# Kernel optimization log

Hardware: AMD Instinct MI355X
Metric: run time of the kernel (lower is better)

## Reference

```python
import jax, jax.numpy as jnp
import numpy as np

L = 8      # num_layers (experts)
N = 8192   # tokens
H = 768    # hidden_dim
I = 1536   # inner = hidden_dim * expansion (2.0)


def setup_inputs() -> dict:
    key = jax.random.key(0)
    k = jax.random.split(key, 6)
    s1 = 1.0 / np.sqrt(H)  # torch nn.Linear default init bound (fan_in)
    s2 = 1.0 / np.sqrt(I)
    return {
        "z": jax.random.normal(k[0], (N, H), dtype=jnp.float32),
        "layer_ids": jax.random.randint(k[1], (N,), 0, L),
        "w1": jax.random.uniform(k[2], (L, H, I), jnp.float32, -s1, s1),
        "b1": jax.random.uniform(k[3], (L, I), jnp.float32, -s1, s1),
        "w2": jax.random.uniform(k[4], (L, I, H), jnp.float32, -s2, s2),
        "b2": jax.random.uniform(k[5], (L, H), jnp.float32, -s2, s2),
    }


def reference(z, layer_ids, w1, b1, w2, b2):
    # Per-token expert MLP: out[n] = z[n] + MLP_{layer_ids[n]}(z[n]).
    # Dense-all-experts formulation (jit-safe, no data-dependent shapes):
    # run every expert on all tokens, then gather each token's own expert row.
    h = jnp.einsum('nh,lhi->lni', z, w1) + b1[:, None, :]       # [L, N, I]
    a = jax.nn.gelu(h, approximate=False)                        # exact erf GELU (torch default)
    y = jnp.einsum('lni,lih->lnh', a, w2) + b2[:, None, :]       # [L, N, H]
    sel = y[layer_ids, jnp.arange(z.shape[0])]                   # [N, H] pick each token's expert
    return z + sel
```

## Files before the change

### kernel.cpp

```cpp
#include <hip/hip_runtime.h>
#include <cstdint>
#include <cstddef>

#define LNUM 8
#define NTOK 8192
#define HDIM 768
#define IDIM 1536

typedef __bf16 bf16x8 __attribute__((ext_vector_type(8)));
typedef float f32x4 __attribute__((ext_vector_type(4)));

__device__ __forceinline__ void gload16(void* lds, const void* gsrc) {
  __builtin_amdgcn_global_load_lds(
      (const __attribute__((address_space(1))) void*)gsrc,
      (__attribute__((address_space(3))) void*)lds, 16, 0, 0);
}

__device__ __forceinline__ float gelu_f(float x) {
  float xx = x * x;
  float u = x * __builtin_fmaf(0.0356774081f, xx, 0.7978845608f);
  float t = __builtin_exp2f(-2.8853900817779268f * u);
  return x * __builtin_amdgcn_rcpf(1.0f + t);
}

__global__ void hist_kernel(const int* __restrict__ lid, int* __restrict__ meta) {
  __shared__ int c[LNUM];
  if (threadIdx.x < LNUM) c[threadIdx.x] = 0;
  __syncthreads();
  int i = blockIdx.x * 256 + threadIdx.x;
  atomicAdd(&c[lid[i]], 1);
  __syncthreads();
  if (threadIdx.x < LNUM) meta[blockIdx.x * LNUM + threadIdx.x] = c[threadIdx.x];
}

__device__ __forceinline__ void tr_cvt_tile(float (*tile)[65], const float* src,
                                            __bf16* dst, int R, int C, int r0,
                                            int c0, int t) {
  int rr = t >> 4, cc = (t & 15) << 2;
  #pragma unroll
  for (int it = 0; it < 4; ++it) {
    float4 v = *(const float4*)&src[(size_t)(r0 + rr + it * 16) * C + c0 + cc];
    tile[rr + it * 16][cc] = v.x;
    tile[rr + it * 16][cc + 1] = v.y;
    tile[rr + it * 16][cc + 2] = v.z;
    tile[rr + it * 16][cc + 3] = v.w;
  }
  __syncthreads();
  int c = t >> 2, rcb = (t & 3) << 3;
  #pragma unroll
  for (int it = 0; it < 2; ++it) {
    int r = rcb + it * 32;
    bf16x8 o;
    #pragma unroll
    for (int j = 0; j < 8; ++j) o[j] = (__bf16)tile[r + j][c];
    *(bf16x8*)&dst[(size_t)(c0 + c) * R + r0 + r] = o;
  }
}

#define NB_SC 32
#define NB_CZ 3072
#define NB_W 2304
__global__ __launch_bounds__(256) void megaprep_kernel(
    const int* __restrict__ lid, const float* __restrict__ z,
    const float* __restrict__ w1, const float* __restrict__ w2,
    int* __restrict__ meta, int* __restrict__ perm, bf16x8* __restrict__ zb,
    __bf16* __restrict__ w1t, __bf16* __restrict__ w2t) {
  __shared__ float tile[64][65];
  __shared__ int lcnt[LNUM], lbase[LNUM];
  int bxid = blockIdx.x;
  int tid = threadIdx.x;
  if (bxid < NB_SC) {
    int b = bxid;
    if (tid < LNUM) {
      lcnt[tid] = 0;
      int base = 0;
      for (int ee = 0; ee < tid; ++ee) {
        int s = 0;
        for (int bb = 0; bb < 32; ++bb) s += meta[bb * LNUM + ee];
        base += s;
      }
      for (int bb = 0; bb < b; ++bb) base += meta[bb * LNUM + tid];
      lbase[tid] = base;
    }
    __syncthreads();
    int i = b * 256 + tid;
    int e = lid[i];
    int r = atomicAdd(&lcnt[e], 1);
    perm[lbase[e] + r] = i;
    if (b == 0 && tid == 0) {
      int o = 0, tt = 0;
      for (int e2 = 0; e2 < LNUM; ++e2) {
        int s = 0;
        for (int bb = 0; bb < 32; ++bb) s += meta[bb * LNUM + e2];
        meta[256 + e2] = o;
        meta[265 + e2] = tt;
        o += s;
        tt += (s + 127) >> 7;
      }
      meta[264] = o;
      meta[273] = tt;
    }
  } else if (bxid < NB_SC + NB_CZ) {
    int i = (bxid - NB_SC) * 256 + tid;
    const float4* zf = (const float4*)z;
    float4 a = zf[i * 2], b4 = zf[i * 2 + 1];
    bf16x8 o;
    o[0] = (__bf16)a.x; o[1] = (__bf16)a.y; o[2] = (__bf16)a.z; o[3] = (__bf16)a.w;
    o[4] = (__bf16)b4.x; o[5] = (__bf16)b4.y; o[6] = (__bf16)b4.z; o[7] = (__bf16)b4.w;
    zb[i] = o;
  } else if (bxid < NB_SC + NB_CZ + NB_W) {
    int idx = bxid - (NB_SC + NB_CZ);
    int e = idx / 288, rem = idx % 288;
    int c0 = (rem % 24) * 64, r0 = (rem / 24) * 64;
    tr_cvt_tile(tile, w1 + (size_t)e * HDIM * IDIM, w1t + (size_t)e * HDIM * IDIM,
                HDIM, IDIM, r0, c0, tid);
  } else {
    int idx = bxid - (NB_SC + NB_CZ + NB_W);
    int e = idx / 288, rem = idx % 288;
    int c0 = (rem % 12) * 64, r0 = (rem / 12) * 64;
    tr_cvt_tile(tile, w2 + (size_t)e * HDIM * IDIM, w2t + (size_t)e * HDIM * IDIM,
                IDIM, HDIM, r0, c0, tid);
  }
}

__global__ __launch_bounds__(512) void gemm1_kernel(
    const __bf16* __restrict__ zb, const __bf16* __restrict__ w1t,
    const float* __restrict__ b1, const int* __restrict__ meta,
    const int* __restrict__ perm, __bf16* __restrict__ act) {
  __shared__ __bf16 As[2][128 * 64];
  __shared__ __bf16 Bs[2][128 * 64];
  const int* offs = meta + 256;
  const int* tiles = meta + 265;
  int nwg = gridDim.x;
  int bid = blockIdx.x;
  int tileid = (bid & 7) * (nwg >> 3) + (bid >> 3);
  int bx = tileid % (IDIM / 128);
  int t = tileid / (IDIM / 128);
  if (t >= tiles[LNUM]) return;
  int e = 0;
  #pragma unroll
  for (int q = 0; q < LNUM - 1; ++q)
    if (t >= tiles[e + 1]) ++e;
  int mtile = t - tiles[e];
  int row0 = offs[e] + (mtile << 7);
  int cntRem = offs[e + 1] - row0;
  if (cntRem > 128) cntRem = 128;
  int n0 = bx << 7;
  int tid = threadIdx.x, lane = tid & 63, wv = tid >> 6;
  int wr = wv >> 2, wc = wv & 3;
  int swz = ((lane & 7) ^ (lane >> 3)) << 3;

  const __bf16* srcA[2];
  const __bf16* srcB[2];
  #pragma unroll
  for (int i = 0; i < 2; ++i) {
    int row = ((wv * 2 + i) << 3) + (lane >> 3);
    int rA = row < cntRem ? row : cntRem - 1;
    int tok = perm[row0 + rA];
    srcA[i] = zb + (size_t)tok * HDIM + swz;
    srcB[i] = w1t + ((size_t)e * IDIM + n0 + row) * HDIM + swz;
  }

  int rswz = (lane & 7) << 3;
  f32x4 acc[4][2] = {};

  #pragma unroll
  for (int i = 0; i < 2; ++i) {
    gload16((char*)As[0] + (((wv * 2 + i)) << 10), srcA[i]);
    gload16((char*)Bs[0] + (((wv * 2 + i)) << 10), srcB[i]);
  }
  __syncthreads();

  int cur = 0;
  for (int kk = 0; kk < HDIM / 64; ++kk) {
    if (kk + 1 < HDIM / 64) {
      #pragma unroll
      for (int i = 0; i < 2; ++i) {
        gload16((char*)As[cur ^ 1] + (((wv * 2 + i)) << 10), srcA[i] + (kk + 1) * 64);
        gload16((char*)Bs[cur ^ 1] + (((wv * 2 + i)) << 10), srcB[i] + (kk + 1) * 64);
      }
    }
    #pragma unroll
    for (int k2 = 0; k2 < 2; ++k2) {
      int kb = (k2 * 32 + ((lane >> 4) << 3)) ^ rswz;
      bf16x8 a[4], b[2];
      #pragma unroll
      for (int mi = 0; mi < 4; ++mi)
        a[mi] = *(const bf16x8*)&As[cur][((wr * 64 + mi * 16 + (lane & 15)) << 6) + kb];
      #pragma unroll
      for (int ni = 0; ni < 2; ++ni)
        b[ni] = *(const bf16x8*)&Bs[cur][((wc * 32 + ni * 16 + (lane & 15)) << 6) + kb];
      #pragma unroll
      for (int mi = 0; mi < 4; ++mi)
        #pragma unroll
        for (int ni = 0; ni < 2; ++ni)
          acc[mi][ni] = __builtin_amdgcn_mfma_f32_16x16x32_bf16(a[mi], b[ni], acc[mi][ni], 0, 0, 0);
    }
    __syncthreads();
    cur ^= 1;
  }

  float bb[2];
  #pragma unroll
  for (int ni = 0; ni < 2; ++ni)
    bb[ni] = b1[e * IDIM + n0 + wc * 32 + ni * 16 + (lane & 15)];

  #pragma unroll
  for (int mi = 0; mi < 4; ++mi) {
    int gr0 = wr * 64 + mi * 16 + ((lane >> 4) << 2);
    #pragma unroll
    for (int r = 0; r < 4; ++r) {
      int g = gr0 + r;
      if (g < cntRem) {
        size_t p = (size_t)(row0 + g);
        #pragma unroll
        for (int ni = 0; ni < 2; ++ni) {
          int col = n0 + wc * 32 + ni * 16 + (lane & 15);
          act[p * IDIM + col] = (__bf16)gelu_f(acc[mi][ni][r] + bb[ni]);
        }
      }
    }
  }
}

__global__ __launch_bounds__(512) void gemm2_kernel(
    const __bf16* __restrict__ act, const __bf16* __restrict__ w2t,
    const float* __restrict__ b2, const float* __restrict__ z,
    const int* __restrict__ meta, const int* __restrict__ perm,
    float* __restrict__ out) {
  __shared__ __bf16 As[2][128 * 64];
  __shared__ __bf16 Bs[2][128 * 64];
  const int* offs = meta + 256;
  const int* tiles = meta + 265;
  int nwg = gridDim.x;
  int bid = blockIdx.x;
  int tileid = (bid & 7) * (nwg >> 3) + (bid >> 3);
  int bx = tileid % (HDIM / 128);
  int t = tileid / (HDIM / 128);
  if (t >= tiles[LNUM]) return;
  int e = 0;
  #pragma unroll
  for (int q = 0; q < LNUM - 1; ++q)
    if (t >= tiles[e + 1]) ++e;
  int mtile = t - tiles[e];
  int row0 = offs[e] + (mtile << 7);
  int cntRem = offs[e + 1] - row0;
  if (cntRem > 128) cntRem = 128;
  int n0 = bx << 7;
  int tid = threadIdx.x, lane = tid & 63, wv = tid >> 6;
  int wr = wv >> 2, wc = wv & 3;
  int swz = ((lane & 7) ^ (lane >> 3)) << 3;

  const __bf16* srcA[2];
  const __bf16* srcB[2];
  #pragma unroll
  for (int i = 0; i < 2; ++i) {
    int row = ((wv * 2 + i) << 3) + (lane >> 3);
    int rA = row < cntRem ? row : cntRem - 1;
    srcA[i] = act + (size_t)(row0 + rA) * IDIM + swz;
    srcB[i] = w2t + ((size_t)e * HDIM + n0 + row) * IDIM + swz;
  }

  int rswz = (lane & 7) << 3;
  f32x4 acc[4][2] = {};

  #pragma unroll
  for (int i = 0; i < 2; ++i) {
    gload16((char*)As[0] + (((wv * 2 + i)) << 10), srcA[i]);
    gload16((char*)Bs[0] + (((wv * 2 + i)) << 10), srcB[i]);
  }
  __syncthreads();

  int cur = 0;
  for (int kk = 0; kk < IDIM / 64; ++kk) {
    if (kk + 1 < IDIM / 64) {
      #pragma unroll
      for (int i = 0; i < 2; ++i) {
        gload16((char*)As[cur ^ 1] + (((wv * 2 + i)) << 10), srcA[i] + (kk + 1) * 64);
        gload16((char*)Bs[cur ^ 1] + (((wv * 2 + i)) << 10), srcB[i] + (kk + 1) * 64);
      }
    }
    #pragma unroll
    for (int k2 = 0; k2 < 2; ++k2) {
      int kb = (k2 * 32 + ((lane >> 4) << 3)) ^ rswz;
      bf16x8 a[4], b[2];
      #pragma unroll
      for (int mi = 0; mi < 4; ++mi)
        a[mi] = *(const bf16x8*)&As[cur][((wr * 64 + mi * 16 + (lane & 15)) << 6) + kb];
      #pragma unroll
      for (int ni = 0; ni < 2; ++ni)
        b[ni] = *(const bf16x8*)&Bs[cur][((wc * 32 + ni * 16 + (lane & 15)) << 6) + kb];
      #pragma unroll
      for (int mi = 0; mi < 4; ++mi)
        #pragma unroll
        for (int ni = 0; ni < 2; ++ni)
          acc[mi][ni] = __builtin_amdgcn_mfma_f32_16x16x32_bf16(a[mi], b[ni], acc[mi][ni], 0, 0, 0);
    }
    __syncthreads();
    cur ^= 1;
  }

  float bb[2];
  #pragma unroll
  for (int ni = 0; ni < 2; ++ni)
    bb[ni] = b2[e * HDIM + n0 + wc * 32 + ni * 16 + (lane & 15)];

  #pragma unroll
  for (int mi = 0; mi < 4; ++mi) {
    int gr0 = wr * 64 + mi * 16 + ((lane >> 4) << 2);
    #pragma unroll
    for (int r = 0; r < 4; ++r) {
      int g = gr0 + r;
      if (g < cntRem) {
        int p = row0 + g;
        int tok = perm[p];
        #pragma unroll
        for (int ni = 0; ni < 2; ++ni) {
          int col = n0 + wc * 32 + ni * 16 + (lane & 15);
          out[(size_t)tok * HDIM + col] =
              z[(size_t)tok * HDIM + col] + acc[mi][ni][r] + bb[ni];
        }
      }
    }
  }
}

extern "C" void kernel_launch(void* const* d_in, const int* in_sizes, int n_in,
                              void* d_out, int out_size, void* d_ws, size_t ws_size,
                              hipStream_t stream) {
  const float* z  = (const float*)d_in[0];
  const int*   lid = (const int*)d_in[1];
  const float* w1 = (const float*)d_in[2];
  const float* b1 = (const float*)d_in[3];
  const float* w2 = (const float*)d_in[4];
  const float* b2 = (const float*)d_in[5];
  float* out = (float*)d_out;
  char* ws = (char*)d_ws;

  int* meta = (int*)ws;
  int* perm = (int*)(ws + 2048);
  __bf16* zb  = (__bf16*)(ws + 2048 + 32768);
  __bf16* w1t = zb + (size_t)NTOK * HDIM;
  __bf16* w2t = w1t + (size_t)LNUM * HDIM * IDIM;
  __bf16* act = w2t + (size_t)LNUM * HDIM * IDIM;

  hist_kernel<<<NTOK / 256, 256, 0, stream>>>(lid, meta);
  megaprep_kernel<<<NB_SC + NB_CZ + 2 * NB_W, 256, 0, stream>>>(
      lid, z, w1, w2, meta, perm, (bf16x8*)zb, w1t, w2t);
  gemm1_kernel<<<(IDIM / 128) * 72, 512, 0, stream>>>(zb, w1t, b1, meta, perm, act);
  gemm2_kernel<<<(HDIM / 128) * 72, 512, 0, stream>>>(act, w2t, b2, z, meta, perm, out);
}
```

Measured before the change: 110.3 us.

## Fold histogram into prep, overlap w2 conversion with gemm1, shrink GEMM tiles

```diff
diff --git a/kernel.cpp b/kernel.cpp
--- a/kernel.cpp
+++ b/kernel.cpp
@@ -21,16 +21,6 @@
   float u = x * __builtin_fmaf(0.0356774081f, xx, 0.7978845608f);
   float t = __builtin_exp2f(-2.8853900817779268f * u);
   return x * __builtin_amdgcn_rcpf(1.0f + t);
-}
-
-__global__ void hist_kernel(const int* __restrict__ lid, int* __restrict__ meta) {
-  __shared__ int c[LNUM];
-  if (threadIdx.x < LNUM) c[threadIdx.x] = 0;
-  __syncthreads();
-  int i = blockIdx.x * 256 + threadIdx.x;
-  atomicAdd(&c[lid[i]], 1);
-  __syncthreads();
-  if (threadIdx.x < LNUM) meta[blockIdx.x * LNUM + threadIdx.x] = c[threadIdx.x];
 }
 
 __device__ __forceinline__ void tr_cvt_tile(float (*tile)[65], const float* src,
@@ -60,46 +50,55 @@
 #define NB_SC 32
 #define NB_CZ 3072
 #define NB_W 2304
-__global__ __launch_bounds__(256) void megaprep_kernel(
+__global__ __launch_bounds__(256) void prep_kernel(
     const int* __restrict__ lid, const float* __restrict__ z,
-    const float* __restrict__ w1, const float* __restrict__ w2,
-    int* __restrict__ meta, int* __restrict__ perm, bf16x8* __restrict__ zb,
-    __bf16* __restrict__ w1t, __bf16* __restrict__ w2t) {
+    const float* __restrict__ w1, int* __restrict__ meta,
+    int* __restrict__ perm, bf16x8* __restrict__ zb, __bf16* __restrict__ w1t) {
   __shared__ float tile[64][65];
-  __shared__ int lcnt[LNUM], lbase[LNUM];
   int bxid = blockIdx.x;
   int tid = threadIdx.x;
   if (bxid < NB_SC) {
-    int b = bxid;
+    __shared__ int ctw[4][LNUM], cbw[4][LNUM];
+    __shared__ int lcnt[LNUM], lbase[LNUM];
+    int b = bxid, wv = tid >> 6;
+    if (tid < 32) {
+      ctw[tid >> 3][tid & 7] = 0;
+      cbw[tid >> 3][tid & 7] = 0;
+    }
+    if (tid < LNUM) lcnt[tid] = 0;
+    __syncthreads();
+    int cut = b << 8;
+    for (int i = tid; i < NTOK; i += 256) {
+      int e = lid[i];
+      atomicAdd(&ctw[wv][e], 1);
+      if (i < cut) atomicAdd(&cbw[wv][e], 1);
+    }
+    __syncthreads();
     if (tid < LNUM) {
-      lcnt[tid] = 0;
-      int base = 0;
-      for (int ee = 0; ee < tid; ++ee) {
-        int s = 0;
-        for (int bb = 0; bb < 32; ++bb) s += meta[bb * LNUM + ee];
-        base += s;
+      int e = tid, o = 0;
+      for (int e2 = 0; e2 < LNUM; ++e2) {
+        int s = ctw[0][e2] + ctw[1][e2] + ctw[2][e2] + ctw[3][e2];
+        if (e2 < e) o += s;
       }
-      for (int bb = 0; bb < b; ++bb) base += meta[bb * LNUM + tid];
-      lbase[tid] = base;
-    }
-    __syncthreads();
-    int i = b * 256 + tid;
+      lbase[e] = o + cbw[0][e] + cbw[1][e] + cbw[2][e] + cbw[3][e];
+    }
+    if (b == 0 && tid == 0) {
+      int o = 0, tt = 0;
+      for (int e2 = 0; e2 < LNUM; ++e2) {
+        int s = ctw[0][e2] + ctw[1][e2] + ctw[2][e2] + ctw[3][e2];
+        meta[e2] = o;
+        meta[9 + e2] = tt;
+        o += s;
+        tt += (s + 127) >> 7;
+      }
+      meta[8] = o;
+      meta[17] = tt;
+    }
+    __syncthreads();
+    int i = (b << 8) + tid;
     int e = lid[i];
     int r = atomicAdd(&lcnt[e], 1);
     perm[lbase[e] + r] = i;
-    if (b == 0 && tid == 0) {
-      int o = 0, tt = 0;
-      for (int e2 = 0; e2 < LNUM; ++e2) {
-        int s = 0;
-        for (int bb = 0; bb < 32; ++bb) s += meta[bb * LNUM + e2];
-        meta[256 + e2] = o;
-        meta[265 + e2] = tt;
-        o += s;
-        tt += (s + 127) >> 7;
-      }
-      meta[264] = o;
-      meta[273] = tt;
-    }
   } else if (bxid < NB_SC + NB_CZ) {
     int i = (bxid - NB_SC) * 256 + tid;
     const float4* zf = (const float4*)z;
@@ -108,34 +107,41 @@
     o[0] = (__bf16)a.x; o[1] = (__bf16)a.y; o[2] = (__bf16)a.z; o[3] = (__bf16)a.w;
     o[4] = (__bf16)b4.x; o[5] = (__bf16)b4.y; o[6] = (__bf16)b4.z; o[7] = (__bf16)b4.w;
     zb[i] = o;
-  } else if (bxid < NB_SC + NB_CZ + NB_W) {
+  } else {
     int idx = bxid - (NB_SC + NB_CZ);
     int e = idx / 288, rem = idx % 288;
     int c0 = (rem % 24) * 64, r0 = (rem / 24) * 64;
     tr_cvt_tile(tile, w1 + (size_t)e * HDIM * IDIM, w1t + (size_t)e * HDIM * IDIM,
                 HDIM, IDIM, r0, c0, tid);
-  } else {
-    int idx = bxid - (NB_SC + NB_CZ + NB_W);
+  }
+}
+
+#define G1NT 24
+#define G1GRID (G1NT * 72)
+__global__ __launch_bounds__(256) void gemm1_kernel(
+    const __bf16* __restrict__ zb, const __bf16* __restrict__ w1t,
+    const float* __restrict__ b1, const int* __restrict__ meta,
+    const int* __restrict__ perm, __bf16* __restrict__ act,
+    const float* __restrict__ w2, __bf16* __restrict__ w2t) {
+  __shared__ __align__(16) char smem[24576];
+  int bid = blockIdx.x;
+  int tid = threadIdx.x;
+  if (bid >= G1GRID) {
+    float (*tile)[65] = (float (*)[65])smem;
+    int idx = bid - G1GRID;
     int e = idx / 288, rem = idx % 288;
     int c0 = (rem % 12) * 64, r0 = (rem / 12) * 64;
     tr_cvt_tile(tile, w2 + (size_t)e * HDIM * IDIM, w2t + (size_t)e * HDIM * IDIM,
                 IDIM, HDIM, r0, c0, tid);
-  }
-}
-
-__global__ __launch_bounds__(512) void gemm1_kernel(
-    const __bf16* __restrict__ zb, const __bf16* __restrict__ w1t,
-    const float* __restrict__ b1, const int* __restrict__ meta,
-    const int* __restrict__ perm, __bf16* __restrict__ act) {
-  __shared__ __bf16 As[2][128 * 64];
-  __shared__ __bf16 Bs[2][128 * 64];
-  const int* offs = meta + 256;
-  const int* tiles = meta + 265;
-  int nwg = gridDim.x;
-  int bid = blockIdx.x;
-  int tileid = (bid & 7) * (nwg >> 3) + (bid >> 3);
-  int bx = tileid % (IDIM / 128);
-  int t = tileid / (IDIM / 128);
+    return;
+  }
+  __bf16* As = (__bf16*)smem;
+  __bf16* Bs = (__bf16*)(smem + 16384);
+  const int* offs = meta;
+  const int* tiles = meta + 9;
+  int tileid = (bid & 7) * (G1GRID >> 3) + (bid >> 3);
+  int bx = tileid % G1NT;
+  int t = tileid / G1NT;
   if (t >= tiles[LNUM]) return;
   int e = 0;
   #pragma unroll
@@ -145,51 +151,47 @@
   int row0 = offs[e] + (mtile << 7);
   int cntRem = offs[e + 1] - row0;
   if (cntRem > 128) cntRem = 128;
-  int n0 = bx << 7;
-  int tid = threadIdx.x, lane = tid & 63, wv = tid >> 6;
-  int wr = wv >> 2, wc = wv & 3;
+  int n0 = bx << 6;
+  int lane = tid & 63, wv = tid >> 6;
+  int wr = wv >> 1, wc = wv & 1;
   int swz = ((lane & 7) ^ (lane >> 3)) << 3;
 
-  const __bf16* srcA[2];
+  const __bf16* srcA[4];
   const __bf16* srcB[2];
   #pragma unroll
-  for (int i = 0; i < 2; ++i) {
-    int row = ((wv * 2 + i) << 3) + (lane >> 3);
+  for (int i = 0; i < 4; ++i) {
+    int row = ((wv * 4 + i) << 3) + (lane >> 3);
     int rA = row < cntRem ? row : cntRem - 1;
     int tok = perm[row0 + rA];
     srcA[i] = zb + (size_t)tok * HDIM + swz;
+  }
+  #pragma unroll
+  for (int i = 0; i < 2; ++i) {
+    int row = ((wv * 2 + i) << 3) + (lane >> 3);
     srcB[i] = w1t + ((size_t)e * IDIM + n0 + row) * HDIM + swz;
   }
 
   int rswz = (lane & 7) << 3;
   f32x4 acc[4][2] = {};
 
-  #pragma unroll
-  for (int i = 0; i < 2; ++i) {
-    gload16((char*)As[0] + (((wv * 2 + i)) << 10), srcA[i]);
-    gload16((char*)Bs[0] + (((wv * 2 + i)) << 10), srcB[i]);
-  }
-  __syncthreads();
-
-  int cur = 0;
   for (int kk = 0; kk < HDIM / 64; ++kk) {
-    if (kk + 1 < HDIM / 64) {
-      #pragma unroll
-      for (int i = 0; i < 2; ++i) {
-        gload16((char*)As[cur ^ 1] + (((wv * 2 + i)) << 10), srcA[i] + (kk + 1) * 64);
-        gload16((char*)Bs[cur ^ 1] + (((wv * 2 + i)) << 10), srcB[i] + (kk + 1) * 64);
-      }
-    }
+    #pragma unroll
+    for (int i = 0; i < 4; ++i)
+      gload16(As + ((wv * 4 + i) << 9), srcA[i] + kk * 64);
+    #pragma unroll
+    for (int i = 0; i < 2; ++i)
+      gload16(Bs + ((wv * 2 + i) << 9), srcB[i] + kk * 64);
+    __syncthreads();
     #pragma unroll
     for (int k2 = 0; k2 < 2; ++k2) {
       int kb = (k2 * 32 + ((lane >> 4) << 3)) ^ rswz;
       bf16x8 a[4], b[2];
       #pragma unroll
       for (int mi = 0; mi < 4; ++mi)
-        a[mi] = *(const bf16x8*)&As[cur][((wr * 64 + mi * 16 + (lane & 15)) << 6) + kb];
+        a[mi] = *(const bf16x8*)&As[((wr * 64 + mi * 16 + (lane & 15)) << 6) + kb];
       #pragma unroll
       for (int ni = 0; ni < 2; ++ni)
-        b[ni] = *(const bf16x8*)&Bs[cur][((wc * 32 + ni * 16 + (lane & 15)) << 6) + kb];
+        b[ni] = *(const bf16x8*)&Bs[((wc * 32 + ni * 16 + (lane & 15)) << 6) + kb];
       #pragma unroll
       for (int mi = 0; mi < 4; ++mi)
         #pragma unroll
@@ -197,7 +199,6 @@
           acc[mi][ni] = __builtin_amdgcn_mfma_f32_16x16x32_bf16(a[mi], b[ni], acc[mi][ni], 0, 0, 0);
     }
     __syncthreads();
-    cur ^= 1;
   }
 
   float bb[2];
@@ -223,20 +224,22 @@
   }
 }
 
-__global__ __launch_bounds__(512) void gemm2_kernel(
+#define G2NT 12
+#define G2GRID (G2NT * 72)
+__global__ __launch_bounds__(256) void gemm2_kernel(
     const __bf16* __restrict__ act, const __bf16* __restrict__ w2t,
     const float* __restrict__ b2, const float* __restrict__ z,
     const int* __restrict__ meta, const int* __restrict__ perm,
     float* __restrict__ out) {
-  __shared__ __bf16 As[2][128 * 64];
-  __shared__ __bf16 Bs[2][128 * 64];
-  const int* offs = meta + 256;
-  const int* tiles = meta + 265;
-  int nwg = gridDim.x;
+  __shared__ __align__(16) char smem[24576];
+  __bf16* As = (__bf16*)smem;
+  __bf16* Bs = (__bf16*)(smem + 16384);
+  const int* offs = meta;
+  const int* tiles = meta + 9;
   int bid = blockIdx.x;
-  int tileid = (bid & 7) * (nwg >> 3) + (bid >> 3);
-  int bx = tileid % (HDIM / 128);
-  int t = tileid / (HDIM / 128);
+  int tileid = (bid & 7) * (G2GRID >> 3) + (bid >> 3);
+  int bx = tileid % G2NT;
+  int t = tileid / G2NT;
   if (t >= tiles[LNUM]) return;
   int e = 0;
   #pragma unroll
@@ -246,50 +249,46 @@
   int row0 = offs[e] + (mtile << 7);
   int cntRem = offs[e + 1] - row0;
   if (cntRem > 128) cntRem = 128;
-  int n0 = bx << 7;
+  int n0 = bx << 6;
   int tid = threadIdx.x, lane = tid & 63, wv = tid >> 6;
-  int wr = wv >> 2, wc = wv & 3;
+  int wr = wv >> 1, wc = wv & 1;
   int swz = ((lane & 7) ^ (lane >> 3)) << 3;
 
-  const __bf16* srcA[2];
+  const __bf16* srcA[4];
   const __bf16* srcB[2];
+  #pragma unroll
+  for (int i = 0; i < 4; ++i) {
+    int row = ((wv * 4 + i) << 3) + (lane >> 3);
+    int rA = row < cntRem ? row : cntRem - 1;
+    srcA[i] = act + (size_t)(row0 + rA) * IDIM + swz;
+  }
   #pragma unroll
   for (int i = 0; i < 2; ++i) {
     int row = ((wv * 2 + i) << 3) + (lane >> 3);
-    int rA = row < cntRem ? row : cntRem - 1;
-    srcA[i] = act + (size_t)(row0 + rA) * IDIM + swz;
     srcB[i] = w2t + ((size_t)e * HDIM + n0 + row) * IDIM + swz;
   }
 
   int rswz = (lane & 7) << 3;
   f32x4 acc[4][2] = {};
 
-  #pragma unroll
-  for (int i = 0; i < 2; ++i) {
-    gload16((char*)As[0] + (((wv * 2 + i)) << 10), srcA[i]);
-    gload16((char*)Bs[0] + (((wv * 2 + i)) << 10), srcB[i]);
-  }
-  __syncthreads();
-
-  int cur = 0;
   for (int kk = 0; kk < IDIM / 64; ++kk) {
-    if (kk + 1 < IDIM / 64) {
-      #pragma unroll
-      for (int i = 0; i < 2; ++i) {
-        gload16((char*)As[cur ^ 1] + (((wv * 2 + i)) << 10), srcA[i] + (kk + 1) * 64);
-        gload16((char*)Bs[cur ^ 1] + (((wv * 2 + i)) << 10), srcB[i] + (kk + 1) * 64);
-      }
-    }
+    #pragma unroll
+    for (int i = 0; i < 4; ++i)
+      gload16(As + ((wv * 4 + i) << 9), srcA[i] + kk * 64);
+    #pragma unroll
+    for (int i = 0; i < 2; ++i)
+      gload16(Bs + ((wv * 2 + i) << 9), srcB[i] + kk * 64);
+    __syncthreads();
     #pragma unroll
     for (int k2 = 0; k2 < 2; ++k2) {
       int kb = (k2 * 32 + ((lane >> 4) << 3)) ^ rswz;
       bf16x8 a[4], b[2];
       #pragma unroll
       for (int mi = 0; mi < 4; ++mi)
-        a[mi] = *(const bf16x8*)&As[cur][((wr * 64 + mi * 16 + (lane & 15)) << 6) + kb];
+        a[mi] = *(const bf16x8*)&As[((wr * 64 + mi * 16 + (lane & 15)) << 6) + kb];
       #pragma unroll
       for (int ni = 0; ni < 2; ++ni)
-        b[ni] = *(const bf16x8*)&Bs[cur][((wc * 32 + ni * 16 + (lane & 15)) << 6) + kb];
+        b[ni] = *(const bf16x8*)&Bs[((wc * 32 + ni * 16 + (lane & 15)) << 6) + kb];
       #pragma unroll
       for (int mi = 0; mi < 4; ++mi)
         #pragma unroll
@@ -297,7 +296,6 @@
           acc[mi][ni] = __builtin_amdgcn_mfma_f32_16x16x32_bf16(a[mi], b[ni], acc[mi][ni], 0, 0, 0);
     }
     __syncthreads();
-    cur ^= 1;
   }
 
   float bb[2];
@@ -344,9 +342,9 @@
   __bf16* w2t = w1t + (size_t)LNUM * HDIM * IDIM;
   __bf16* act = w2t + (size_t)LNUM * HDIM * IDIM;
 
-  hist_kernel<<<NTOK / 256, 256, 0, stream>>>(lid, meta);
-  megaprep_kernel<<<NB_SC + NB_CZ + 2 * NB_W, 256, 0, stream>>>(
-      lid, z, w1, w2, meta, perm, (bf16x8*)zb, w1t, w2t);
-  gemm1_kernel<<<(IDIM / 128) * 72, 512, 0, stream>>>(zb, w1t, b1, meta, perm, act);
-  gemm2_kernel<<<(HDIM / 128) * 72, 512, 0, stream>>>(act, w2t, b2, z, meta, perm, out);
-}
+  prep_kernel<<<NB_SC + NB_CZ + NB_W, 256, 0, stream>>>(
+      lid, z, w1, meta, perm, (bf16x8*)zb, w1t);
+  gemm1_kernel<<<G1GRID + NB_W, 256, 0, stream>>>(zb, w1t, b1, meta, perm, act,
+                                                  w2, w2t);
+  gemm2_kernel<<<G2GRID, 256, 0, stream>>>(act, w2t, b2, z, meta, perm, out);
+}
```

Result: faster. 106.0 us (-3.9%).
